# Kernel optimization log

Measured on AMD Instinct MI355X. Metric: run time of the kernel, lower is better.

## Reference

```python
import jax, jax.numpy as jnp
import numpy as np

B, L = 4, 8192
IN_CH, OUT_CH = 1, 1
H = 64               # d_model
NSTATE = 16          # d_state
DBLK = 4             # number of residual blocks
DCONV = 16
EXPAND = 2
DINNER = EXPAND * H              # 128
HEADDIM = H // 4                 # 16
NHEADS = DINNER // HEADDIM       # 8
CONV_DIM = DINNER + 2 * NSTATE   # 160 (ngroups=1)
D_IN_PROJ = 2 * DINNER + 2 * NSTATE + NHEADS  # 296
CHUNK = 128


def setup_inputs():
    key = jax.random.key(0)
    ks = jax.random.split(key, 12)
    rn = lambda k, shape, s: (jax.random.normal(k, shape) * s).astype(jnp.float32)
    x = rn(ks[0], (B, L, IN_CH), 1.0)
    w_in = rn(ks[1], (H, IN_CH), 1.0)
    w_out = rn(ks[2], (OUT_CH, H), 1.0 / np.sqrt(H))
    in_proj_w = rn(ks[3], (DBLK, D_IN_PROJ, H), 1.0 / np.sqrt(H))
    conv_w = rn(ks[4], (DBLK, CONV_DIM, DCONV), 1.0 / np.sqrt(DCONV))
    conv_b = rn(ks[5], (DBLK, CONV_DIM), 0.02)
    dt = jnp.exp(jax.random.uniform(ks[6], (DBLK, NHEADS)) * (np.log(0.1) - np.log(1e-3)) + np.log(1e-3))
    dt_bias = (dt + jnp.log(-jnp.expm1(-dt))).astype(jnp.float32)  # inverse softplus
    A_log = jnp.log(jax.random.uniform(ks[7], (DBLK, NHEADS), minval=1.0, maxval=16.0)).astype(jnp.float32)
    D_skip = jnp.ones((DBLK, NHEADS), jnp.float32)
    init_states = rn(ks[8], (DBLK, NHEADS, HEADDIM, NSTATE), 0.01)
    norm_w = jnp.ones((DBLK, DINNER), jnp.float32)
    out_proj_w = rn(ks[9], (DBLK, H, DINNER), 1.0 / np.sqrt(DINNER))
    mlp_w = rn(ks[10], (DBLK, H, H), 1.0 / np.sqrt(H))
    mlp_b = jnp.zeros((DBLK, H), jnp.float32)
    return {"x": x, "w_in": w_in, "w_out": w_out, "in_proj_w": in_proj_w,
            "conv_w": conv_w, "conv_b": conv_b, "dt_bias": dt_bias, "A_log": A_log,
            "D_skip": D_skip, "init_states": init_states, "norm_w": norm_w,
            "out_proj_w": out_proj_w, "mlp_w": mlp_w, "mlp_b": mlp_b}


def segsum(a):
    # a: (..., q) -> (..., q, q); seg[i, j] = sum_{k=j+1..i} a[k] on lower triangle (diag=0), exp->0 above
    q = a.shape[-1]
    cs = jnp.cumsum(a, axis=-1)
    seg = cs[..., :, None] - cs[..., None, :]
    mask = jnp.tril(jnp.ones((q, q), dtype=bool))
    return jnp.where(mask, seg, -1e30)


def ssd(X, dA, Bm, Cm, init_state):
    # Chunked SSD (Mamba2 paper). X: (b,l,h,p) = x*dt, dA: (b,l,h), Bm/Cm: (b,l,n), init_state: (b,h,p,n)
    b, l, h, p = X.shape
    c = l // CHUNK
    X = X.reshape(b, c, CHUNK, h, p)
    Bm = Bm.reshape(b, c, CHUNK, NSTATE)
    Cm = Cm.reshape(b, c, CHUNK, NSTATE)
    A = dA.reshape(b, c, CHUNK, h).transpose(0, 3, 1, 2)  # (b,h,c,q)
    A_cs = jnp.cumsum(A, axis=-1)
    # intra-chunk (diagonal blocks)
    Lm = jnp.exp(segsum(A))  # (b,h,c,q,q)
    Y_diag = jnp.einsum('bcln,bcsn,bhcls,bcshp->bclhp', Cm, Bm, Lm, X)
    # per-chunk final states
    decay_states = jnp.exp(A_cs[..., -1:] - A_cs)  # (b,h,c,q)
    states = jnp.einsum('bcln,bhcl,bclhp->bchpn', Bm, decay_states, X)
    states = jnp.concatenate([init_state[:, None], states], axis=1)  # (b,c+1,h,p,n)
    # inter-chunk recurrence (vectorized via segsum over chunk decays)
    decay_chunk = jnp.exp(segsum(jnp.pad(A_cs[..., -1], ((0, 0), (0, 0), (1, 0)))))  # (b,h,c+1,c+1)
    new_states = jnp.einsum('bhzc,bchpn->bzhpn', decay_chunk, states)
    prev_states = new_states[:, :-1]  # state entering each chunk
    state_decay = jnp.exp(A_cs)
    Y_off = jnp.einsum('bcln,bchpn,bhcl->bclhp', Cm, prev_states, state_decay)
    return (Y_diag + Y_off).reshape(b, l, h, p)


def mamba2(u, w_inp, cw, cb, dtb, alog, dskip, istate, nw, w_outp):
    b, l, _ = u.shape
    zxbcdt = jnp.einsum('bld,ed->ble', u, w_inp)  # (b,l,296)
    z = zxbcdt[..., :DINNER]
    xBC = zxbcdt[..., DINNER:DINNER + CONV_DIM]
    dt = jax.nn.softplus(zxbcdt[..., DINNER + CONV_DIM:] + dtb)  # (b,l,h)
    # causal depthwise conv over seq + silu
    xBC = jax.lax.conv_general_dilated(
        xBC.transpose(0, 2, 1), cw[:, None, :], (1,), [(DCONV - 1, 0)],
        feature_group_count=CONV_DIM, dimension_numbers=('NCH', 'OIH', 'NCH'))
    xBC = jax.nn.silu(xBC + cb[None, :, None]).transpose(0, 2, 1)
    xs = xBC[..., :DINNER]
    Bm = xBC[..., DINNER:DINNER + NSTATE]
    Cm = xBC[..., DINNER + NSTATE:]
    A = -jnp.exp(alog)  # (h,)
    xh = xs.reshape(b, l, NHEADS, HEADDIM)
    init = jnp.broadcast_to(istate, (b,) + istate.shape)
    y = ssd(xh * dt[..., None], dt * A, Bm, Cm, init)
    y = y + xh * dskip[None, None, :, None]  # D skip
    y = y.reshape(b, l, DINNER)
    # gated RMSNorm: norm(y * silu(z)) * weight
    y = y * jax.nn.silu(z)
    y = y * jax.lax.rsqrt(jnp.mean(y * y, axis=-1, keepdims=True) + 1e-5) * nw
    return jnp.einsum('ble,de->bld', y, w_outp)


def reference(x, w_in, w_out, in_proj_w, conv_w, conv_b, dt_bias, A_log,
              D_skip, init_states, norm_w, out_proj_w, mlp_w, mlp_b):
    h = jnp.einsum('bli,hi->blh', x, w_in)
    for i in range(DBLK):
        y = mamba2(h, in_proj_w[i], conv_w[i], conv_b[i], dt_bias[i], A_log[i],
                   D_skip[i], init_states[i], norm_w[i], out_proj_w[i])
        t = y / jnp.sqrt(1.0 + y * y)  # TanhApprox
        y = jnp.einsum('blh,oh->blo', t, mlp_w[i]) + mlp_b[i]
        h = h + y  # residual
    return jnp.einsum('blh,oh->blo', h, w_out)
```

## Files before the change

kernel.cpp:

```cpp
#include <hip/hip_runtime.h>
#include <math.h>

#define NB 4
#define SEQ 8192
#define NT (NB*SEQ)
#define HDIM 64
#define NST 16
#define NBLK 4
#define KCONV 16
#define DIN 128
#define PDIM 16
#define NH 8
#define CDIM 160
#define EPROJ 296
#define CH 128
#define NC 64

typedef __attribute__((ext_vector_type(8))) short short8;
typedef __attribute__((ext_vector_type(4))) float f32x4;

__device__ __forceinline__ float sigf(float x){ return 1.0f/(1.0f+__expf(-x)); }

__device__ __forceinline__ unsigned short bf16r(float f){
  unsigned int u = __float_as_uint(f);
  u = (u + 0x7fffu + ((u >> 16) & 1u)) >> 16;
  return (unsigned short)u;
}
__device__ __forceinline__ unsigned int pk_bf16(float a, float b){
  return (unsigned int)bf16r(a) | ((unsigned int)bf16r(b) << 16);
}
__device__ __forceinline__ float bf16f(unsigned short h){
  return __uint_as_float(((unsigned int)h) << 16);
}

__global__ __launch_bounds__(256) void k_init_h(const float* __restrict__ x, const float* __restrict__ w_in,
                                                float* __restrict__ h){
  int i = blockIdx.x*256 + threadIdx.x;
  int t = i >> 6, d = i & 63;
  h[i] = x[t]*w_in[d];
}

__global__ __launch_bounds__(256) void k_wsplit(const float* __restrict__ w,
                                                unsigned short* __restrict__ whi,
                                                unsigned short* __restrict__ wlo){
  int i = blockIdx.x*256 + threadIdx.x;
  if(i < NBLK*EPROJ*HDIM){
    float f = w[i];
    unsigned short hi = bf16r(f);
    float fh = bf16f(hi);
    whi[i] = hi;
    wlo[i] = bf16r(f - fh);
  }
}

__global__ __launch_bounds__(256) void k_inproj(const float* __restrict__ h,
                                                const unsigned short* __restrict__ whi,
                                                const unsigned short* __restrict__ wlo,
                                                unsigned short* __restrict__ zxz,
                                                float* __restrict__ zxc){
  int tid = threadIdx.x;
  int lane = tid & 63, wid = tid >> 6;
  int quad = lane >> 4, lq = lane & 15;
  int t0 = blockIdx.x*64 + wid*16;

  const float* hp = h + (size_t)(t0+lq)*HDIM;
  short8 bh[2], bl[2];
#pragma unroll
  for(int kb=0;kb<2;kb++){
    float4 f0 = *(const float4*)(hp + kb*32 + quad*8);
    float4 f1 = *(const float4*)(hp + kb*32 + quad*8 + 4);
    float v[8] = {f0.x,f0.y,f0.z,f0.w,f1.x,f1.y,f1.z,f1.w};
#pragma unroll
    for(int j=0;j<8;j++){
      unsigned short hi = bf16r(v[j]);
      bh[kb][j] = (short)hi;
      bl[kb][j] = (short)bf16r(v[j] - bf16f(hi));
    }
  }

  for(int et=0; et<19; et++){
    int e_a = et*16 + lq;
    int ec = (e_a < EPROJ) ? e_a : (EPROJ-1);
    const unsigned short* wh = whi + (size_t)ec*HDIM + quad*8;
    const unsigned short* wl = wlo + (size_t)ec*HDIM + quad*8;
    short8 ah0 = *(const short8*)wh;
    short8 ah1 = *(const short8*)(wh + 32);
    short8 al0 = *(const short8*)wl;
    short8 al1 = *(const short8*)(wl + 32);
    f32x4 acc = {0.f,0.f,0.f,0.f};
    acc = __builtin_amdgcn_mfma_f32_16x16x32_bf16(ah0, bh[0], acc, 0, 0, 0);
    acc = __builtin_amdgcn_mfma_f32_16x16x32_bf16(ah1, bh[1], acc, 0, 0, 0);
    acc = __builtin_amdgcn_mfma_f32_16x16x32_bf16(ah0, bl[0], acc, 0, 0, 0);
    acc = __builtin_amdgcn_mfma_f32_16x16x32_bf16(ah1, bl[1], acc, 0, 0, 0);
    acc = __builtin_amdgcn_mfma_f32_16x16x32_bf16(al0, bh[0], acc, 0, 0, 0);
    acc = __builtin_amdgcn_mfma_f32_16x16x32_bf16(al1, bh[1], acc, 0, 0, 0);
#pragma unroll
    for(int r=0;r<4;r++){
      int e = et*16 + quad*4 + r;
      if(e < 128)        zxz[(size_t)e*NT + t0 + lq] = bf16r(acc[r]);
      else if(e < EPROJ) zxc[(size_t)(e-128)*NT + t0 + lq] = acc[r];
    }
  }
}

__global__ __launch_bounds__(512) void k_mid(const float* __restrict__ zxc,
                                             const float* __restrict__ cw, const float* __restrict__ cb,
                                             const float* __restrict__ dtb, const float* __restrict__ alog,
                                             unsigned short* __restrict__ xbc, float* __restrict__ dt,
                                             float* __restrict__ acs, float* __restrict__ asum,
                                             float* __restrict__ S){
  __shared__ unsigned short XhT[128][136];
  __shared__ unsigned short XlT[128][136];
  __shared__ unsigned short BhT[16][136];
  __shared__ unsigned short BlT[16][136];
  __shared__ float dtl[8][128];
  __shared__ float wle[8][128];

  int bc = blockIdx.x;
  int c = bc & 63, b = bc >> 6;
  int t0 = b*SEQ + c*CH;
  int tid = threadIdx.x;

  for(int it=0; it<5; it++){
    int G = tid + it*512;
    int ch = G >> 4;
    int sg = (G & 15) * 8;
    const float* p = zxc + (size_t)ch*NT + t0 + sg - 16;
    float buf[24];
    if(c == 0 && sg < 16){
#pragma unroll
      for(int j=0;j<24;j++){
        int l = sg - 16 + j;
        buf[j] = (l >= 0) ? p[j] : 0.f;
      }
    } else {
#pragma unroll
      for(int q4=0;q4<6;q4++){
        float4 f = *(const float4*)(p + q4*4);
        buf[q4*4+0]=f.x; buf[q4*4+1]=f.y; buf[q4*4+2]=f.z; buf[q4*4+3]=f.w;
      }
    }
    float wv[16];
#pragma unroll
    for(int k=0;k<16;k++) wv[k] = cw[ch*KCONV+k];
    float bias = cb[ch];
    unsigned short hs[8];
#pragma unroll
    for(int s=0;s<8;s++){
      float acc = bias;
#pragma unroll
      for(int k=0;k<16;k++) acc += wv[k]*buf[s+1+k];
      float r = acc * sigf(acc);
      unsigned short hi = bf16r(r);
      unsigned short lo = bf16r(r - bf16f(hi));
      hs[s] = hi;
      if(ch < 128){ XhT[ch][sg+s] = hi; XlT[ch][sg+s] = lo; }
      else if(ch < 144){ BhT[ch-128][sg+s] = hi; BlT[ch-128][sg+s] = lo; }
    }
    uint4 pk;
    pk.x = (unsigned int)hs[0] | ((unsigned int)hs[1] << 16);
    pk.y = (unsigned int)hs[2] | ((unsigned int)hs[3] << 16);
    pk.z = (unsigned int)hs[4] | ((unsigned int)hs[5] << 16);
    pk.w = (unsigned int)hs[6] | ((unsigned int)hs[7] << 16);
    *(uint4*)(xbc + (size_t)ch*NT + t0 + sg) = pk;
  }
#pragma unroll
  for(int k=0;k<2;k++){
    int idx = tid + k*512;
    int hh = idx >> 7, s = idx & 127;
    float raw = zxc[(size_t)(CDIM + hh)*NT + t0 + s] + dtb[hh];
    float v = (raw > 20.f) ? raw : log1pf(__expf(raw));
    dtl[hh][s] = v;
    dt[(size_t)hh*NT + t0 + s] = v;
  }
  __syncthreads();

  int lane = tid & 63, wid = tid >> 6;
  {
    int hh = wid;
    float A = -__expf(alog[hh]);
    float d0 = dtl[hh][2*lane], d1 = dtl[hh][2*lane+1];
    float v0 = d0*A, v1 = d1*A;
    float s = v0 + v1;
    for(int off=1; off<64; off<<=1){
      float o = __shfl_up(s, off);
      if(lane >= off) s += o;
    }
    float tot = __shfl(s, 63);
    float excl = s - (v0+v1);
    float a0 = excl+v0, a1 = excl+v0+v1;
    *(float2*)&acs[(size_t)hh*NT + t0 + 2*lane] = make_float2(a0, a1);
    if(lane == 63) asum[(size_t)bc*NH + hh] = tot;
    wle[hh][2*lane]   = d0*__expf(tot - a0);
    wle[hh][2*lane+1] = d1*__expf(tot - a1);
  }
  __syncthreads();

  {
    int hh = wid;
    int lq = lane & 15, quad = lane >> 4;
    f32x4 acc = {0.f,0.f,0.f,0.f};
#pragma unroll
    for(int kb=0;kb<4;kb++){
      int k0 = kb*32 + quad*8;
      short8 xh = *(const short8*)&XhT[hh*16 + lq][k0];
      short8 xl = *(const short8*)&XlT[hh*16 + lq][k0];
      short8 ah, al;
#pragma unroll
      for(int j=0;j<8;j++){
        float xv = bf16f((unsigned short)xh[j]) + bf16f((unsigned short)xl[j]);
        float pw = xv * wle[hh][k0 + j];
        unsigned short hi = bf16r(pw);
        ah[j] = (short)hi;
        al[j] = (short)bf16r(pw - bf16f(hi));
      }
      short8 bh = *(const short8*)&BhT[lq][k0];
      short8 bl = *(const short8*)&BlT[lq][k0];
      acc = __builtin_amdgcn_mfma_f32_16x16x32_bf16(ah, bh, acc, 0, 0, 0);
      acc = __builtin_amdgcn_mfma_f32_16x16x32_bf16(ah, bl, acc, 0, 0, 0);
      acc = __builtin_amdgcn_mfma_f32_16x16x32_bf16(al, bh, acc, 0, 0, 0);
    }
    float* Sp = S + ((size_t)bc*NH + hh)*256;
#pragma unroll
    for(int r=0;r<4;r++) Sp[(quad*4 + r)*16 + lq] = acc[r];
  }
}

__global__ __launch_bounds__(64) void k_scan(const float* __restrict__ S, const float* __restrict__ asum,
                                             const float* __restrict__ init, float* __restrict__ prev){
  int q  = blockIdx.x & 3;
  int hh = (blockIdx.x >> 2) & 7;
  int b  = blockIdx.x >> 5;
  int el = q*64 + threadIdx.x;
  const size_t cs = (size_t)NH*256;
  const float* Sp = S + ((size_t)(b*NC)*NH + hh)*256 + el;
  float* Pp = prev + ((size_t)(b*NC)*NH + hh)*256 + el;
  const float* ap = asum + (size_t)(b*NC)*NH + hh;
  float r = init[hh*256 + el];
  float s0 = Sp[0], s1 = Sp[cs], s2 = Sp[2*cs], s3 = Sp[3*cs];
  for(int c=0;c<NC;c+=4){
    Pp[(size_t)c*cs] = r;
    r = __expf(ap[(size_t)c*NH])*r + s0;
    s0 = (c+4 < NC) ? Sp[(size_t)(c+4)*cs] : 0.f;
    Pp[(size_t)(c+1)*cs] = r;
    r = __expf(ap[(size_t)(c+1)*NH])*r + s1;
    s1 = (c+5 < NC) ? Sp[(size_t)(c+5)*cs] : 0.f;
    Pp[(size_t)(c+2)*cs] = r;
    r = __expf(ap[(size_t)(c+2)*NH])*r + s2;
    s2 = (c+6 < NC) ? Sp[(size_t)(c+6)*cs] : 0.f;
    Pp[(size_t)(c+3)*cs] = r;
    r = __expf(ap[(size_t)(c+3)*NH])*r + s3;
    s3 = (c+7 < NC) ? Sp[(size_t)(c+7)*cs] : 0.f;
  }
}

__global__ __launch_bounds__(1024) void k_tail(const unsigned short* __restrict__ xbc,
                                               const unsigned short* __restrict__ zxz,
                                               const float* __restrict__ dt, const float* __restrict__ acs,
                                               const float* __restrict__ prev, const float* __restrict__ dskip,
                                               const float* __restrict__ nw, const float* __restrict__ opw,
                                               const float* __restrict__ mw, const float* __restrict__ mb,
                                               float* __restrict__ h,
                                               int last, const float* __restrict__ wout,
                                               float* __restrict__ out){
  __shared__ __align__(16) unsigned char sm[151840];
  unsigned short* Bb   = (unsigned short*)(sm);
  unsigned short* Cb   = (unsigned short*)(sm + 6144);
  unsigned short* XbT  = (unsigned short*)(sm + 12288);
  unsigned short* P0   = (unsigned short*)(sm + 55296);
  unsigned short* P1   = (unsigned short*)(sm + 98304);
  float* Al  = (float*)(sm + 141312);
  float* Dtl = (float*)(sm + 145408);
  float* nwl = (float*)(sm + 149504);
  float* mbl = (float*)(sm + 150016);
  unsigned short* zbuf = (unsigned short*)(sm + 150272);
  float* ssl  = (float*)(sm + 150304);
  float* outb = (float*)(sm + 151328);
  unsigned short* Zb = XbT;
  unsigned short* Wo = P0;
  unsigned short* Wm = P0 + 64*136;
  unsigned short* Yn = P1;
  unsigned short* Tt = P1;

  int bc = blockIdx.x;
  int c = bc & 63, b = bc >> 6;
  int t0 = b*SEQ + c*CH;
  int tid = threadIdx.x, lane = tid & 63, wid = tid >> 6;
  int quad = lane >> 4, lq = lane & 15;
  int hgrp = wid >> 3;
  int strip = (wid & 7)*16;

#pragma unroll
  for(int k=0;k<4;k++){
    int idx = tid + k*1024;
    int ch = idx >> 7, s = idx & 127;
    unsigned short f = xbc[(size_t)(DIN+ch)*NT + t0 + s];
    if(ch < 16) Bb[s*24 + ch] = f;
    else        Cb[s*24 + ch-16] = f;
  }
#pragma unroll
  for(int k=0;k<4;k++){
    int fi = tid + k*1024;
    int p = fi >> 5, s4 = fi & 31;
    uint2 xu = *(const uint2*)&xbc[(size_t)p*NT + t0 + s4*4];
    float4 dv = *(const float4*)&dt[(size_t)(p>>4)*NT + t0 + s4*4];
    float x0 = bf16f((unsigned short)(xu.x & 0xffffu));
    float x1 = bf16f((unsigned short)(xu.x >> 16));
    float x2 = bf16f((unsigned short)(xu.y & 0xffffu));
    float x3 = bf16f((unsigned short)(xu.y >> 16));
    *(unsigned int*)&XbT[p*168 + s4*4]   = pk_bf16(x0*dv.x, x1*dv.y);
    *(unsigned int*)&XbT[p*168 + s4*4+2] = pk_bf16(x2*dv.z, x3*dv.w);
  }
#pragma unroll
  for(int k=0;k<2;k++){
    int idx = tid + k*1024;
    int hh = idx >> 8, rest = idx & 255;
    int p = rest >> 4, n = rest & 15;
    XbT[(hh*16+p)*168 + 128 + n] = bf16r(prev[((size_t)bc*NH + hh)*256 + rest]);
  }
#pragma unroll
  for(int k=0;k<2;k++){
    int idx = tid + k*1024;
    if(idx < 1536){
      int p = idx / 12, cc = idx - p*12;
      *(unsigned int*)&XbT[p*168 + 144 + 2*cc] = 0u;
    }
  }
  {
    int hh = tid >> 7, s = tid & 127;
    Al[hh*128+s]  = acs[(size_t)hh*NT + t0 + s];
    Dtl[hh*128+s] = dt[(size_t)hh*NT + t0 + s];
  }
  if(tid < 128) nwl[tid] = nw[tid];
  else if(tid < 192) mbl[tid-128] = mb[tid-128];
  else if(tid < 208) zbuf[tid-192] = 0;
  {
    unsigned short* Pg = hgrp ? P1 : P0;
#pragma unroll
    for(int k=0;k<3;k++){
      int idx = lane + k*64;
      int rr = idx / 12, cc = idx - rr*12;
      *(unsigned int*)&Pg[(strip+rr)*168 + 144 + 2*cc] = 0u;
    }
  }
  __syncthreads();

  short8 afr;
  {
    int row = strip + lq;
    const unsigned short* ap = (quad < 2) ? &Cb[row*24 + quad*8] : zbuf;
    afr = *(const short8*)ap;
  }
  f32x4 sc[8];
#pragma unroll
  for(int nt=0;nt<8;nt++){
    const unsigned short* bp = (quad < 2) ? &Bb[(nt*16+lq)*24 + quad*8] : zbuf;
    short8 bfr = *(const short8*)bp;
    f32x4 acc = {0.f,0.f,0.f,0.f};
    sc[nt] = __builtin_amdgcn_mfma_f32_16x16x32_bf16(afr, bfr, acc, 0, 0, 0);
  }

  unsigned short* Pg = hgrp ? P1 : P0;
  f32x4 accv[4];
  for(int j=0;j<4;j++){
    int hh2 = hgrp*4 + j;
    const float* Alh = Al + hh2*128;
    float alr[4];
#pragma unroll
    for(int r=0;r<4;r++) alr[r] = Alh[strip + quad*4 + r];
#pragma unroll
    for(int nt=0;nt<8;nt++){
      int col = nt*16 + lq;
      float alc = Alh[col];
#pragma unroll
      for(int r=0;r<4;r++){
        int row = strip + quad*4 + r;
        float p = sc[nt][r] * __expf(alr[r] - alc);
        p = (col <= row) ? p : 0.f;
        Pg[row*168 + col] = bf16r(p);
      }
    }
    {
      int n = lane & 15, rg = lane >> 4;
#pragma unroll
      for(int rr=0;rr<4;rr++){
        int row = strip + rg*4 + rr;
        float ea = __expf(Alh[row]);
        Pg[row*168 + 128 + n] = bf16r(bf16f(Cb[row*24+n]) * ea);
      }
    }
    f32x4 acc2 = {0.f,0.f,0.f,0.f};
#pragma unroll
    for(int ks=0;ks<5;ks++){
      short8 bfr = *(const short8*)&XbT[(hh2*16+lq)*168 + ks*32 + quad*8];
      short8 af  = *(const short8*)&Pg[(strip+lq)*168 + ks*32 + quad*8];
      acc2 = __builtin_amdgcn_mfma_f32_16x16x32_bf16(af, bfr, acc2, 0, 0, 0);
    }
    const float* Dth = Dtl + hh2*128;
    float Dk = dskip[hh2];
#pragma unroll
    for(int r=0;r<4;r++){
      int l = strip + quad*4 + r;
      float xdt = bf16f(XbT[(hh2*16+lq)*168 + l]);
      float dtv = fmaxf(Dth[l], 1e-30f);
      acc2[r] += Dk * xdt * __frcp_rn(dtv);
    }
    accv[j] = acc2;
  }
  __syncthreads();

#pragma unroll
  for(int k=0;k<4;k++){
    int fi = tid + k*1024;
    int p = fi >> 5, s4 = fi & 31;
    uint2 zu = *(const uint2*)&zxz[(size_t)p*NT + t0 + s4*4];
    *(unsigned int*)&Zb[p*136 + s4*4]   = zu.x;
    *(unsigned int*)&Zb[p*136 + s4*4+2] = zu.y;
  }
#pragma unroll
  for(int k=0;k<2;k++){
    int fi = tid + k*1024;
    int n = fi >> 5, k4 = fi & 31;
    float4 wv = *(const float4*)&opw[(size_t)n*DIN + k4*4];
    *(unsigned int*)&Wo[n*136 + k4*4]   = pk_bf16(wv.x, wv.y);
    *(unsigned int*)&Wo[n*136 + k4*4+2] = pk_bf16(wv.z, wv.w);
  }
  {
    int fi = tid;
    int n = fi >> 4, k4 = fi & 15;
    float4 wv = *(const float4*)&mw[(size_t)n*HDIM + k4*4];
    *(unsigned int*)&Wm[n*72 + k4*4]   = pk_bf16(wv.x, wv.y);
    *(unsigned int*)&Wm[n*72 + k4*4+2] = pk_bf16(wv.z, wv.w);
  }
  __syncthreads();

  float part[4] = {0.f,0.f,0.f,0.f};
#pragma unroll
  for(int j=0;j<4;j++){
    int ch = (hgrp*4+j)*16 + lq;
    float nwv = nwl[ch];
#pragma unroll
    for(int r=0;r<4;r++){
      int l = strip + quad*4 + r;
      float zv = bf16f(Zb[ch*136 + l]);
      float g = zv * sigf(zv);
      float yv = accv[j][r] * g;
      part[r] += yv*yv;
      Yn[l*136 + ch] = bf16r(yv * nwv);
    }
  }
#pragma unroll
  for(int r=0;r<4;r++){
    part[r] += __shfl_xor(part[r],1); part[r] += __shfl_xor(part[r],2);
    part[r] += __shfl_xor(part[r],4); part[r] += __shfl_xor(part[r],8);
  }
  if(lq == 0){
#pragma unroll
    for(int r=0;r<4;r++) ssl[hgrp*128 + strip + quad*4 + r] = part[r];
  }
  __syncthreads();

  float rms_[4];
#pragma unroll
  for(int r=0;r<4;r++){
    int l = strip + quad*4 + r;
    rms_[r] = rsqrtf((ssl[l] + ssl[128+l])*(1.0f/128.0f) + 1e-5f);
  }
  short8 afk[4];
#pragma unroll
  for(int ks=0;ks<4;ks++) afk[ks] = *(const short8*)&Yn[(strip+lq)*136 + ks*32 + quad*8];
  f32x4 aco[2];
#pragma unroll
  for(int ntl=0;ntl<2;ntl++){ aco[ntl] = (f32x4){0.f,0.f,0.f,0.f}; }
#pragma unroll
  for(int ntl=0;ntl<2;ntl++){
    int nt = hgrp*2 + ntl;
#pragma unroll
    for(int ks=0;ks<4;ks++){
      short8 bfr = *(const short8*)&Wo[(nt*16+lq)*136 + ks*32 + quad*8];
      aco[ntl] = __builtin_amdgcn_mfma_f32_16x16x32_bf16(afk[ks], bfr, aco[ntl], 0, 0, 0);
    }
  }
  __syncthreads();
#pragma unroll
  for(int ntl=0;ntl<2;ntl++){
    int nt = hgrp*2 + ntl;
#pragma unroll
    for(int r=0;r<4;r++){
      int l = strip + quad*4 + r;
      float o = aco[ntl][r] * rms_[r];
      Tt[l*136 + nt*16+lq] = bf16r(o * rsqrtf(1.0f + o*o));
    }
  }
  __syncthreads();

  f32x4 acm[2];
#pragma unroll
  for(int ntl=0;ntl<2;ntl++){ acm[ntl] = (f32x4){0.f,0.f,0.f,0.f}; }
#pragma unroll
  for(int ks=0;ks<2;ks++){
    short8 af = *(const short8*)&Tt[(strip+lq)*136 + ks*32 + quad*8];
#pragma unroll
    for(int ntl=0;ntl<2;ntl++){
      int nt = hgrp*2 + ntl;
      short8 bfr = *(const short8*)&Wm[(nt*16+lq)*72 + ks*32 + quad*8];
      acm[ntl] = __builtin_amdgcn_mfma_f32_16x16x32_bf16(af, bfr, acm[ntl], 0, 0, 0);
    }
  }
  if(!last){
#pragma unroll
    for(int ntl=0;ntl<2;ntl++){
      int nt = hgrp*2 + ntl;
#pragma unroll
      for(int r=0;r<4;r++){
        int l = strip + quad*4 + r;
        int d = nt*16 + lq;
        size_t gi = (size_t)(t0+l)*HDIM + d;
        h[gi] += acm[ntl][r] + mbl[d];
      }
    }
  } else {
    float ps[4] = {0.f,0.f,0.f,0.f};
#pragma unroll
    for(int ntl=0;ntl<2;ntl++){
      int nt = hgrp*2 + ntl;
      int d = nt*16 + lq;
      float wo = wout[d];
      float bias = mbl[d];
#pragma unroll
      for(int r=0;r<4;r++){
        int l = strip + quad*4 + r;
        size_t gi = (size_t)(t0+l)*HDIM + d;
        float hn = h[gi] + acm[ntl][r] + bias;
        ps[r] += hn * wo;
      }
    }
#pragma unroll
    for(int r=0;r<4;r++){
      ps[r] += __shfl_xor(ps[r],1); ps[r] += __shfl_xor(ps[r],2);
      ps[r] += __shfl_xor(ps[r],4); ps[r] += __shfl_xor(ps[r],8);
    }
    if(hgrp == 1 && lq == 0){
#pragma unroll
      for(int r=0;r<4;r++) outb[strip + quad*4 + r] = ps[r];
    }
    __syncthreads();
    if(hgrp == 0 && lq == 0){
#pragma unroll
      for(int r=0;r<4;r++){
        int l = strip + quad*4 + r;
        out[t0 + l] = ps[r] + outb[l];
      }
    }
  }
}

extern "C" void kernel_launch(void* const* d_in, const int* in_sizes, int n_in,
                              void* d_out, int out_size, void* d_ws, size_t ws_size,
                              hipStream_t stream){
  const float* x          = (const float*)d_in[0];
  const float* w_in       = (const float*)d_in[1];
  const float* w_out      = (const float*)d_in[2];
  const float* in_proj_w  = (const float*)d_in[3];
  const float* conv_w     = (const float*)d_in[4];
  const float* conv_b     = (const float*)d_in[5];
  const float* dt_bias    = (const float*)d_in[6];
  const float* A_log      = (const float*)d_in[7];
  const float* D_skip     = (const float*)d_in[8];
  const float* init_st    = (const float*)d_in[9];
  const float* norm_w     = (const float*)d_in[10];
  const float* out_proj_w = (const float*)d_in[11];
  const float* mlp_w      = (const float*)d_in[12];
  const float* mlp_b      = (const float*)d_in[13];
  float* out = (float*)d_out;

  float* ws = (float*)d_ws;
  float* h    = ws; ws += (size_t)NT*HDIM;
  unsigned short* zxz = (unsigned short*)ws; ws += (size_t)(128*NT)/2;
  float* zxc  = ws; ws += (size_t)168*NT;
  unsigned short* xbc = (unsigned short*)ws; ws += (size_t)(CDIM*NT)/2;
  float* dt   = ws; ws += (size_t)NH*NT;
  float* acs  = ws; ws += (size_t)NH*NT;
  float* asum = ws; ws += (size_t)NB*NC*NH;
  float* S    = ws; ws += (size_t)NB*NC*NH*256;
  float* prev = ws; ws += (size_t)NB*NC*NH*256;
  unsigned short* whi = (unsigned short*)ws; ws += (size_t)(NBLK*EPROJ*HDIM)/2;
  unsigned short* wlo = (unsigned short*)ws; ws += (size_t)(NBLK*EPROJ*HDIM)/2;

  k_init_h<<<(NT*HDIM)/256, 256, 0, stream>>>(x, w_in, h);
  k_wsplit<<<(NBLK*EPROJ*HDIM + 255)/256, 256, 0, stream>>>(in_proj_w, whi, wlo);
  for(int i=0;i<NBLK;i++){
    k_inproj<<<NT/64, 256, 0, stream>>>(h, whi + (size_t)i*EPROJ*HDIM,
                                        wlo + (size_t)i*EPROJ*HDIM, zxz, zxc);
    k_mid   <<<NB*NC, 512, 0, stream>>>(zxc, conv_w + i*CDIM*KCONV, conv_b + i*CDIM,
                                        dt_bias + i*NH, A_log + i*NH,
                                        xbc, dt, acs, asum, S);
    k_scan  <<<NB*NH*4, 64, 0, stream>>>(S, asum, init_st + i*NH*256, prev);
    k_tail  <<<NB*NC, 1024, 0, stream>>>(xbc, zxz, dt, acs, prev, D_skip + i*NH,
                                         norm_w + i*DIN, out_proj_w + i*HDIM*DIN,
                                         mlp_w + i*HDIM*HDIM, mlp_b + i*HDIM, h,
                                         (i == NBLK-1) ? 1 : 0, w_out, out);
  }
}
```

Measured before the change: 362.5 us.

## Skip upper-triangle tiles in tail, prefetch weights, precompute chunk decays, fuse init

Several unrelated changes land together. The tail kernel now skips the score MFMA and the P-matrix fill for tiles above the causal diagonal, zero-fills those regions once up front, and reassigns wave strips to balance the work. The in-projection loop software-prefetches the next weight tile. The chunk decay exp is computed in k_mid so k_scan preloads multipliers without exp. The two init kernels are merged into one launch, and some LDS reads are vectorized. These changes trade register pressure from the prefetch and the 64-entry array for less wasted compute and launch overhead.

```diff
diff --git a/kernel.cpp b/kernel.cpp
--- a/kernel.cpp
+++ b/kernel.cpp
@@ -33,23 +33,26 @@
   return __uint_as_float(((unsigned int)h) << 16);
 }
 
-__global__ __launch_bounds__(256) void k_init_h(const float* __restrict__ x, const float* __restrict__ w_in,
-                                                float* __restrict__ h){
-  int i = blockIdx.x*256 + threadIdx.x;
-  int t = i >> 6, d = i & 63;
-  h[i] = x[t]*w_in[d];
-}
-
-__global__ __launch_bounds__(256) void k_wsplit(const float* __restrict__ w,
-                                                unsigned short* __restrict__ whi,
-                                                unsigned short* __restrict__ wlo){
-  int i = blockIdx.x*256 + threadIdx.x;
-  if(i < NBLK*EPROJ*HDIM){
-    float f = w[i];
-    unsigned short hi = bf16r(f);
-    float fh = bf16f(hi);
-    whi[i] = hi;
-    wlo[i] = bf16r(f - fh);
+__global__ __launch_bounds__(256) void k_init(const float* __restrict__ x, const float* __restrict__ w_in,
+                                              float* __restrict__ h,
+                                              const float* __restrict__ w,
+                                              unsigned short* __restrict__ whi,
+                                              unsigned short* __restrict__ wlo){
+  int bi = blockIdx.x;
+  const int HB = (NT*HDIM)/256;
+  if(bi < HB){
+    int i = bi*256 + threadIdx.x;
+    int t = i >> 6, d = i & 63;
+    h[i] = x[t]*w_in[d];
+  } else {
+    int i = (bi - HB)*256 + threadIdx.x;
+    if(i < NBLK*EPROJ*HDIM){
+      float f = w[i];
+      unsigned short hi = bf16r(f);
+      float fh = bf16f(hi);
+      whi[i] = hi;
+      wlo[i] = bf16r(f - fh);
+    }
   }
 }
 
@@ -78,15 +81,25 @@
     }
   }
 
+  const unsigned short* wh0 = whi + (size_t)lq*HDIM + quad*8;
+  const unsigned short* wl0 = wlo + (size_t)lq*HDIM + quad*8;
+  short8 ah0 = *(const short8*)wh0;
+  short8 ah1 = *(const short8*)(wh0 + 32);
+  short8 al0 = *(const short8*)wl0;
+  short8 al1 = *(const short8*)(wl0 + 32);
+
   for(int et=0; et<19; et++){
-    int e_a = et*16 + lq;
-    int ec = (e_a < EPROJ) ? e_a : (EPROJ-1);
-    const unsigned short* wh = whi + (size_t)ec*HDIM + quad*8;
-    const unsigned short* wl = wlo + (size_t)ec*HDIM + quad*8;
-    short8 ah0 = *(const short8*)wh;
-    short8 ah1 = *(const short8*)(wh + 32);
-    short8 al0 = *(const short8*)wl;
-    short8 al1 = *(const short8*)(wl + 32);
+    short8 nh0 = ah0, nh1 = ah1, nl0 = al0, nl1 = al1;
+    if(et < 18){
+      int e_a = (et+1)*16 + lq;
+      int ec = (e_a < EPROJ) ? e_a : (EPROJ-1);
+      const unsigned short* wh = whi + (size_t)ec*HDIM + quad*8;
+      const unsigned short* wl = wlo + (size_t)ec*HDIM + quad*8;
+      nh0 = *(const short8*)wh;
+      nh1 = *(const short8*)(wh + 32);
+      nl0 = *(const short8*)wl;
+      nl1 = *(const short8*)(wl + 32);
+    }
     f32x4 acc = {0.f,0.f,0.f,0.f};
     acc = __builtin_amdgcn_mfma_f32_16x16x32_bf16(ah0, bh[0], acc, 0, 0, 0);
     acc = __builtin_amdgcn_mfma_f32_16x16x32_bf16(ah1, bh[1], acc, 0, 0, 0);
@@ -100,6 +113,7 @@
       if(e < 128)        zxz[(size_t)e*NT + t0 + lq] = bf16r(acc[r]);
       else if(e < EPROJ) zxc[(size_t)(e-128)*NT + t0 + lq] = acc[r];
     }
+    ah0 = nh0; ah1 = nh1; al0 = nl0; al1 = nl1;
   }
 }
 
@@ -179,7 +193,8 @@
   {
     int hh = wid;
     float A = -__expf(alog[hh]);
-    float d0 = dtl[hh][2*lane], d1 = dtl[hh][2*lane+1];
+    float2 dd = *(const float2*)&dtl[hh][2*lane];
+    float d0 = dd.x, d1 = dd.y;
     float v0 = d0*A, v1 = d1*A;
     float s = v0 + v1;
     for(int off=1; off<64; off<<=1){
@@ -190,7 +205,7 @@
     float excl = s - (v0+v1);
     float a0 = excl+v0, a1 = excl+v0+v1;
     *(float2*)&acs[(size_t)hh*NT + t0 + 2*lane] = make_float2(a0, a1);
-    if(lane == 63) asum[(size_t)bc*NH + hh] = tot;
+    if(lane == 63) asum[(size_t)bc*NH + hh] = __expf(tot);
     wle[hh][2*lane]   = d0*__expf(tot - a0);
     wle[hh][2*lane+1] = d1*__expf(tot - a1);
   }
@@ -205,11 +220,14 @@
       int k0 = kb*32 + quad*8;
       short8 xh = *(const short8*)&XhT[hh*16 + lq][k0];
       short8 xl = *(const short8*)&XlT[hh*16 + lq][k0];
+      float4 w0 = *(const float4*)&wle[hh][k0];
+      float4 w1 = *(const float4*)&wle[hh][k0+4];
+      float wv8[8] = {w0.x,w0.y,w0.z,w0.w,w1.x,w1.y,w1.z,w1.w};
       short8 ah, al;
 #pragma unroll
       for(int j=0;j<8;j++){
         float xv = bf16f((unsigned short)xh[j]) + bf16f((unsigned short)xl[j]);
-        float pw = xv * wle[hh][k0 + j];
+        float pw = xv * wv8[j];
         unsigned short hi = bf16r(pw);
         ah[j] = (short)hi;
         al[j] = (short)bf16r(pw - bf16f(hi));
@@ -226,7 +244,7 @@
   }
 }
 
-__global__ __launch_bounds__(64) void k_scan(const float* __restrict__ S, const float* __restrict__ asum,
+__global__ __launch_bounds__(64) void k_scan(const float* __restrict__ S, const float* __restrict__ easum,
                                              const float* __restrict__ init, float* __restrict__ prev){
   int q  = blockIdx.x & 3;
   int hh = (blockIdx.x >> 2) & 7;
@@ -235,21 +253,25 @@
   const size_t cs = (size_t)NH*256;
   const float* Sp = S + ((size_t)(b*NC)*NH + hh)*256 + el;
   float* Pp = prev + ((size_t)(b*NC)*NH + hh)*256 + el;
-  const float* ap = asum + (size_t)(b*NC)*NH + hh;
+  const float* ap = easum + (size_t)(b*NC)*NH + hh;
+  float e[NC];
+#pragma unroll
+  for(int c=0;c<NC;c++) e[c] = ap[(size_t)c*NH];
   float r = init[hh*256 + el];
   float s0 = Sp[0], s1 = Sp[cs], s2 = Sp[2*cs], s3 = Sp[3*cs];
+#pragma unroll
   for(int c=0;c<NC;c+=4){
     Pp[(size_t)c*cs] = r;
-    r = __expf(ap[(size_t)c*NH])*r + s0;
+    r = e[c]*r + s0;
     s0 = (c+4 < NC) ? Sp[(size_t)(c+4)*cs] : 0.f;
     Pp[(size_t)(c+1)*cs] = r;
-    r = __expf(ap[(size_t)(c+1)*NH])*r + s1;
+    r = e[c+1]*r + s1;
     s1 = (c+5 < NC) ? Sp[(size_t)(c+5)*cs] : 0.f;
     Pp[(size_t)(c+2)*cs] = r;
-    r = __expf(ap[(size_t)(c+2)*NH])*r + s2;
+    r = e[c+2]*r + s2;
     s2 = (c+6 < NC) ? Sp[(size_t)(c+6)*cs] : 0.f;
     Pp[(size_t)(c+3)*cs] = r;
-    r = __expf(ap[(size_t)(c+3)*NH])*r + s3;
+    r = e[c+3]*r + s3;
     s3 = (c+7 < NC) ? Sp[(size_t)(c+7)*cs] : 0.f;
   }
 }
@@ -288,7 +310,9 @@
   int tid = threadIdx.x, lane = tid & 63, wid = tid >> 6;
   int quad = lane >> 4, lq = lane & 15;
   int hgrp = wid >> 3;
-  int strip = (wid & 7)*16;
+  int wr7 = wid & 7;
+  int widr = (wr7 < 4) ? wr7 : (11 - wr7);
+  int strip = widr*16;
 
 #pragma unroll
   for(int k=0;k<4;k++){
@@ -335,12 +359,17 @@
   else if(tid < 192) mbl[tid-128] = mb[tid-128];
   else if(tid < 208) zbuf[tid-192] = 0;
   {
-    unsigned short* Pg = hgrp ? P1 : P0;
+    unsigned short* Pgz = hgrp ? P1 : P0;
 #pragma unroll
     for(int k=0;k<3;k++){
       int idx = lane + k*64;
       int rr = idx / 12, cc = idx - rr*12;
-      *(unsigned int*)&Pg[(strip+rr)*168 + 144 + 2*cc] = 0u;
+      *(unsigned int*)&Pgz[(strip+rr)*168 + 144 + 2*cc] = 0u;
+    }
+    int zc0 = (widr+1)*16;
+    int nu  = (7 - widr)*8;
+    for(int u = lane>>4; u < nu; u += 4){
+      *(unsigned int*)&Pgz[(strip+(lane&15))*168 + zc0 + 2*u] = 0u;
     }
   }
   __syncthreads();
@@ -354,10 +383,13 @@
   f32x4 sc[8];
 #pragma unroll
   for(int nt=0;nt<8;nt++){
-    const unsigned short* bp = (quad < 2) ? &Bb[(nt*16+lq)*24 + quad*8] : zbuf;
-    short8 bfr = *(const short8*)bp;
     f32x4 acc = {0.f,0.f,0.f,0.f};
-    sc[nt] = __builtin_amdgcn_mfma_f32_16x16x32_bf16(afr, bfr, acc, 0, 0, 0);
+    if(nt <= widr){
+      const unsigned short* bp = (quad < 2) ? &Bb[(nt*16+lq)*24 + quad*8] : zbuf;
+      short8 bfr = *(const short8*)bp;
+      acc = __builtin_amdgcn_mfma_f32_16x16x32_bf16(afr, bfr, acc, 0, 0, 0);
+    }
+    sc[nt] = acc;
   }
 
   unsigned short* Pg = hgrp ? P1 : P0;
@@ -370,14 +402,16 @@
     for(int r=0;r<4;r++) alr[r] = Alh[strip + quad*4 + r];
 #pragma unroll
     for(int nt=0;nt<8;nt++){
-      int col = nt*16 + lq;
-      float alc = Alh[col];
-#pragma unroll
-      for(int r=0;r<4;r++){
-        int row = strip + quad*4 + r;
-        float p = sc[nt][r] * __expf(alr[r] - alc);
-        p = (col <= row) ? p : 0.f;
-        Pg[row*168 + col] = bf16r(p);
+      if(nt <= widr){
+        int col = nt*16 + lq;
+        float alc = Alh[col];
+#pragma unroll
+        for(int r=0;r<4;r++){
+          int row = strip + quad*4 + r;
+          float p = sc[nt][r] * __expf(alr[r] - alc);
+          p = (col <= row) ? p : 0.f;
+          Pg[row*168 + col] = bf16r(p);
+        }
       }
     }
     {
@@ -587,8 +621,7 @@
   unsigned short* whi = (unsigned short*)ws; ws += (size_t)(NBLK*EPROJ*HDIM)/2;
   unsigned short* wlo = (unsigned short*)ws; ws += (size_t)(NBLK*EPROJ*HDIM)/2;
 
-  k_init_h<<<(NT*HDIM)/256, 256, 0, stream>>>(x, w_in, h);
-  k_wsplit<<<(NBLK*EPROJ*HDIM + 255)/256, 256, 0, stream>>>(in_proj_w, whi, wlo);
+  k_init<<<(NT*HDIM)/256 + (NBLK*EPROJ*HDIM)/256, 256, 0, stream>>>(x, w_in, h, in_proj_w, whi, wlo);
   for(int i=0;i<NBLK;i++){
     k_inproj<<<NT/64, 256, 0, stream>>>(h, whi + (size_t)i*EPROJ*HDIM,
                                         wlo + (size_t)i*EPROJ*HDIM, zxz, zxc);
```

After: 354.6 us. 2.2% less time.
